# Kernel tuning notes

Hardware: AMD Instinct MI355X
Metric: run time of the kernel (lower is better)

## Reference

```python
import jax, jax.numpy as jnp
import numpy as np

N_NODES = 100000
N_SUPPORTS = 3
N_EDGES = 500000
D_IN = 128
D_OUT = 128


def setup_inputs() -> dict:
    key = jax.random.key(0)
    k1, k2, k3, k4, k5 = jax.random.split(key, 5)
    x = jax.random.normal(k1, (N_NODES, D_IN), dtype=jnp.float32)
    # glorot-ish scale for weights
    W = jax.random.normal(k2, (N_SUPPORTS, D_IN, D_OUT), dtype=jnp.float32) * np.sqrt(2.0 / (D_IN + D_OUT)).astype(np.float32)
    edge_src = jax.random.randint(k3, (N_SUPPORTS, N_EDGES), 0, N_NODES, dtype=jnp.int32)
    edge_dst = jax.random.randint(k4, (N_SUPPORTS, N_EDGES), 0, N_NODES, dtype=jnp.int32)
    edge_val = jax.random.uniform(k5, (N_SUPPORTS, N_EDGES), dtype=jnp.float32)
    return {"x": x, "W": W, "edge_src": edge_src, "edge_dst": edge_dst, "edge_val": edge_val}


def reference(x, W, edge_src, edge_dst, edge_val):
    """HMGConvolution forward (adj_power=1, multi_weight, no attention/reweight).

    x:        [N, Din] dense node features
    W:        [S, Din, Dout] per-support weights
    edge_src: [S, E] source node ids of each adjacency (COO)
    edge_dst: [S, E] destination node ids
    edge_val: [S, E] adjacency values
    Returns relu(sum_s  A_s @ (x @ W_s))  -> [N, Dout]
    """
    n_nodes = x.shape[0]
    # dense transform per support: [S, N, Dout]
    pre_sup = jnp.einsum('nd,sde->sne', x, W)

    def spmm(pre_s, src, dst, val):
        # messages gathered from source nodes, scaled by edge weight
        msgs = val[:, None] * pre_s[src]  # [E, Dout]
        return jax.ops.segment_sum(msgs, dst, num_segments=n_nodes)  # [N, Dout]

    supports = jax.vmap(spmm)(pre_sup, edge_src, edge_dst, edge_val)  # [S, N, Dout]
    return jax.nn.relu(jnp.sum(supports, axis=0))
```

## Files before the change

### kernel.cpp

```cpp
#include <hip/hip_runtime.h>

#define DIN 128
#define DOUT 128
#define EPB 4096
#define BKT 512
#define PACK_BITS 19
#define SRCG_MASK ((1u << PACK_BITS) - 1u)

typedef __attribute__((ext_vector_type(8))) short short8;
typedef __attribute__((ext_vector_type(4))) float f32x4;
typedef __attribute__((ext_vector_type(8))) unsigned short ushort8;

__device__ __forceinline__ unsigned short f2bf(float f) {
  unsigned int u = __float_as_uint(f);
  u += 0x7fffu + ((u >> 16) & 1u);
  return (unsigned short)(u >> 16);
}


__global__ __launch_bounds__(256) void wconvert(const float* __restrict__ W,
                                                unsigned short* __restrict__ wT) {
  __shared__ unsigned short buf[128][136];
  const int s = blockIdx.x;
  const float* Ws = W + (size_t)s * DIN * DOUT;
  unsigned short* wts = wT + (size_t)s * DIN * DOUT;
  const int tid = threadIdx.x;
#pragma unroll
  for (int i = 0; i < 16; ++i) {
    int e = tid + i * 256;
    int k = e >> 5, c = (e & 31) * 4;
    float4 v = *reinterpret_cast<const float4*>(&Ws[(size_t)k * DOUT + c]);
    buf[c][k] = f2bf(v.x); buf[c + 1][k] = f2bf(v.y);
    buf[c + 2][k] = f2bf(v.z); buf[c + 3][k] = f2bf(v.w);
  }
  __syncthreads();
#pragma unroll
  for (int i = 0; i < 8; ++i) {
    int e = tid + i * 256;
    int r = e >> 4, c = (e & 15) * 8;
    *reinterpret_cast<ushort8*>(&wts[(size_t)r * DIN + c]) =
        *reinterpret_cast<const ushort8*>(&buf[r][c]);
  }
}


__global__ __launch_bounds__(256) void gemm_mfma(const float* __restrict__ x,
                                                 const unsigned short* __restrict__ wT,
                                                 unsigned short* __restrict__ pre,
                                                 int n_nodes, int n_sup) {
  __shared__ unsigned short cst[128][136];

  const int tid = threadIdx.x;
  const int lane = tid & 63;
  const int w = tid >> 6;
  const int row0 = blockIdx.x * 128;
  const int alr = lane & 15;
  const int akg = lane >> 4;

  short8 afrag[4][2];
#pragma unroll
  for (int kc = 0; kc < 4; ++kc)
#pragma unroll
    for (int mt = 0; mt < 2; ++mt) {
      int gr = row0 + w * 32 + mt * 16 + alr;
      short8 a = {0, 0, 0, 0, 0, 0, 0, 0};
      if (gr < n_nodes) {
        const float4* p =
            reinterpret_cast<const float4*>(&x[(size_t)gr * DIN + kc * 32 + akg * 8]);
        float4 v0 = p[0];
        float4 v1 = p[1];
        a[0] = (short)f2bf(v0.x); a[1] = (short)f2bf(v0.y);
        a[2] = (short)f2bf(v0.z); a[3] = (short)f2bf(v0.w);
        a[4] = (short)f2bf(v1.x); a[5] = (short)f2bf(v1.y);
        a[6] = (short)f2bf(v1.z); a[7] = (short)f2bf(v1.w);
      }
      afrag[kc][mt] = a;
    }

  for (int s = 0; s < n_sup; ++s) {
    const unsigned short* wts = wT + (size_t)s * DIN * DOUT;

    f32x4 acc[2][8];
#pragma unroll
    for (int mt = 0; mt < 2; ++mt)
#pragma unroll
      for (int nt = 0; nt < 8; ++nt) acc[mt][nt] = (f32x4){0.f, 0.f, 0.f, 0.f};

#pragma unroll
    for (int kc = 0; kc < 4; ++kc) {
      short8 bfrag[8];
#pragma unroll
      for (int nt = 0; nt < 8; ++nt)
        bfrag[nt] = *reinterpret_cast<const short8*>(
            &wts[(size_t)(nt * 16 + alr) * DIN + kc * 32 + akg * 8]);
#pragma unroll
      for (int mt = 0; mt < 2; ++mt)
#pragma unroll
        for (int nt = 0; nt < 8; ++nt)
          acc[mt][nt] = __builtin_amdgcn_mfma_f32_16x16x32_bf16(
              afrag[kc][mt], bfrag[nt], acc[mt][nt], 0, 0, 0);
    }

    __syncthreads();
#pragma unroll
    for (int mt = 0; mt < 2; ++mt)
#pragma unroll
      for (int nt = 0; nt < 8; ++nt)
#pragma unroll
        for (int q = 0; q < 4; ++q)
          cst[w * 32 + mt * 16 + akg * 4 + q][nt * 16 + alr] = f2bf(acc[mt][nt][q]);
    __syncthreads();

    unsigned short* ps = pre + (size_t)s * n_nodes * DOUT;
#pragma unroll
    for (int i = 0; i < 8; ++i) {
      int e = tid + i * 256;
      int r = e >> 4;
      int c = (e & 15) * 8;
      int gr = row0 + r;
      if (gr < n_nodes)
        *reinterpret_cast<ushort8*>(&ps[(size_t)gr * DOUT + c]) =
            *reinterpret_cast<const ushort8*>(&cst[r][c]);
    }
  }
}


__global__ __launch_bounds__(256) void gemm_xw(const float* __restrict__ x,
                                               const float* __restrict__ W,
                                               float* __restrict__ pre,
                                               int n_nodes) {
  __shared__ float xsf[128][33];
  __shared__ float wtf[32][129];
  const float* Ws = W + (size_t)blockIdx.y * DIN * DOUT;
  float* pres = pre + (size_t)blockIdx.y * n_nodes * DOUT;
  const int tid = threadIdx.x;
  const int row0 = blockIdx.x * 128;
  const int tcol = tid & 15;
  const int trow = tid >> 4;
  float acc[8][8];
#pragma unroll
  for (int i = 0; i < 8; ++i)
#pragma unroll
    for (int j = 0; j < 8; ++j) acc[i][j] = 0.f;
#pragma unroll 1
  for (int kk = 0; kk < DIN; kk += 32) {
#pragma unroll
    for (int i = 0; i < 4; ++i) {
      int e = tid + i * 256;
      int r = e >> 3, c = (e & 7) * 4;
      int gr = row0 + r;
      float4 v = make_float4(0.f, 0.f, 0.f, 0.f);
      if (gr < n_nodes)
        v = *reinterpret_cast<const float4*>(&x[(size_t)gr * DIN + kk + c]);
      xsf[r][c] = v.x; xsf[r][c + 1] = v.y; xsf[r][c + 2] = v.z; xsf[r][c + 3] = v.w;
    }
#pragma unroll
    for (int i = 0; i < 4; ++i) {
      int e = tid + i * 256;
      int k = e >> 5, c = (e & 31) * 4;
      float4 v = *reinterpret_cast<const float4*>(&Ws[(size_t)(kk + k) * DOUT + c]);
      wtf[k][c] = v.x; wtf[k][c + 1] = v.y; wtf[k][c + 2] = v.z; wtf[k][c + 3] = v.w;
    }
    __syncthreads();
#pragma unroll 4
    for (int k = 0; k < 32; ++k) {
      float a[8], b[8];
#pragma unroll
      for (int i = 0; i < 8; ++i) a[i] = xsf[trow * 8 + i][k];
#pragma unroll
      for (int j = 0; j < 8; ++j) b[j] = wtf[k][tcol + 16 * j];
#pragma unroll
      for (int i = 0; i < 8; ++i)
#pragma unroll
        for (int j = 0; j < 8; ++j) acc[i][j] = fmaf(a[i], b[j], acc[i][j]);
    }
    __syncthreads();
  }
#pragma unroll
  for (int i = 0; i < 8; ++i) {
    int gr = row0 + trow * 8 + i;
    if (gr < n_nodes) {
#pragma unroll
      for (int j = 0; j < 8; ++j)
        pres[(size_t)gr * DOUT + tcol + 16 * j] = acc[i][j];
    }
  }
}


__global__ __launch_bounds__(256) void bucket_count(const int* __restrict__ dst_all,
                                                    int* __restrict__ bucket_cnt, int TE) {
  __shared__ int cnt[256];
  const int tid = threadIdx.x;
  cnt[tid] = 0;
  __syncthreads();
  const int beg = blockIdx.x * EPB;
  const int end = min(beg + EPB, TE);
  for (int i = beg + tid; i < end; i += 256) atomicAdd(&cnt[dst_all[i] >> 9], 1);
  __syncthreads();
  int c = cnt[tid];
  if (c) atomicAdd(&bucket_cnt[tid], c);
}

__global__ __launch_bounds__(256) void bucket_scan(const int* __restrict__ bucket_cnt,
                                                   int* __restrict__ bucket_base,
                                                   int* __restrict__ bucket_cursor,
                                                   int NB, int TE) {
  __shared__ int tmp[256];
  const int tid = threadIdx.x;
  int v = (tid < NB) ? bucket_cnt[tid] : 0;
  tmp[tid] = v;
  __syncthreads();
#pragma unroll
  for (int d = 1; d < 256; d <<= 1) {
    int t = (tid >= d) ? tmp[tid - d] : 0;
    __syncthreads();
    tmp[tid] += t;
    __syncthreads();
  }
  int excl = tmp[tid] - v;
  if (tid < NB) {
    bucket_base[tid] = excl;
    bucket_cursor[tid] = excl;
  }
  if (tid == 0) bucket_base[NB] = TE;
}

__global__ __launch_bounds__(256) void partition_edges(const int* __restrict__ src_all,
                                                       const int* __restrict__ dst_all,
                                                       const float* __restrict__ val_all,
                                                       int* __restrict__ bucket_cursor,
                                                       int2* __restrict__ part,
                                                       int TE, int n_nodes, int n_edges) {
  __shared__ int cnt[256];
  __shared__ int base_l[256];
  const int tid = threadIdx.x;
  const int beg = blockIdx.x * EPB;
  const int end = min(beg + EPB, TE);

  cnt[tid] = 0;
  __syncthreads();
  for (int i = beg + tid; i < end; i += 256) atomicAdd(&cnt[dst_all[i] >> 9], 1);
  __syncthreads();

  int c = cnt[tid];
  int mybase = (c > 0) ? atomicAdd(&bucket_cursor[tid], c) : 0;
  __syncthreads();
  base_l[tid] = mybase;
  cnt[tid] = 0;
  __syncthreads();

  for (int i = beg + tid; i < end; i += 256) {
    int d = dst_all[i];
    int b = d >> 9;
    int r = atomicAdd(&cnt[b], 1);
    int s = i / n_edges;
    unsigned key = (unsigned)(s * n_nodes + src_all[i]) |
                   ((unsigned)(d & (BKT - 1)) << PACK_BITS);
    part[base_l[b] + r] = make_int2((int)key, __float_as_int(val_all[i]));
  }
}

__global__ __launch_bounds__(256) void csr_build(const int2* __restrict__ part,
                                                 const int* __restrict__ bucket_base,
                                                 int2* __restrict__ csr,
                                                 int* __restrict__ row_off,
                                                 int n_nodes, int TE) {
  __shared__ int cnt[BKT];
  __shared__ int off_s[BKT];
  __shared__ int tmp[256];
  const int b = blockIdx.x;
  const int tid = threadIdx.x;
  const int bb = bucket_base[b];
  const int be = bucket_base[b + 1];

  cnt[tid] = 0;
  cnt[tid + 256] = 0;
  __syncthreads();
  for (int j = bb + tid; j < be; j += 256)
    atomicAdd(&cnt[((unsigned)part[j].x) >> PACK_BITS], 1);
  __syncthreads();

  int s2 = cnt[2 * tid] + cnt[2 * tid + 1];
  tmp[tid] = s2;
  __syncthreads();
#pragma unroll
  for (int d = 1; d < 256; d <<= 1) {
    int t = (tid >= d) ? tmp[tid - d] : 0;
    __syncthreads();
    tmp[tid] += t;
    __syncthreads();
  }
  int excl2 = tmp[tid] - s2;
  off_s[2 * tid] = excl2;
  off_s[2 * tid + 1] = excl2 + cnt[2 * tid];
  __syncthreads();

#pragma unroll
  for (int k = tid; k < BKT; k += 256) {
    int node = b * BKT + k;
    if (node < n_nodes) row_off[node] = bb + off_s[k];
  }
  cnt[tid] = off_s[tid];
  cnt[tid + 256] = off_s[tid + 256];
  __syncthreads();

  for (int j = bb + tid; j < be; j += 256) {
    int2 e = part[j];
    int dl = ((unsigned)e.x) >> PACK_BITS;
    int p = bb + atomicAdd(&cnt[dl], 1);
    csr[p] = e;
  }
  if (b == 0 && tid == 0) row_off[n_nodes] = TE;
}


__global__ __launch_bounds__(256) void spmm_gather8(const unsigned short* __restrict__ pre,
                                                    const int2* __restrict__ csr,
                                                    const int* __restrict__ row_off,
                                                    float* __restrict__ out, int n_nodes) {
  const int lane = threadIdx.x & 63;
  const int g = lane >> 3;
  const int t = lane & 7;
  const int wave = blockIdx.x * (blockDim.x >> 6) + (threadIdx.x >> 6);
  const int nwaves = gridDim.x * (blockDim.x >> 6);

  for (int n = wave; n < n_nodes; n += nwaves) {
    const int beg = row_off[n];
    const int end = row_off[n + 1];
    float acc[16];
#pragma unroll
    for (int k = 0; k < 16; ++k) acc[k] = 0.f;

    for (int j = beg + g; j < end; j += 8) {
      const int2 e = csr[j];
      const float v = __int_as_float(e.y);
      const unsigned srcg = ((unsigned)e.x) & SRCG_MASK;
      const ushort8* pr =
          reinterpret_cast<const ushort8*>(&pre[(size_t)srcg * DOUT + t * 16]);
      ushort8 p0 = pr[0];
      ushort8 p1 = pr[1];
#pragma unroll
      for (int k = 0; k < 8; ++k) {
        acc[k]     = fmaf(v, __uint_as_float((unsigned int)(unsigned short)p0[k] << 16), acc[k]);
        acc[8 + k] = fmaf(v, __uint_as_float((unsigned int)(unsigned short)p1[k] << 16), acc[8 + k]);
      }
    }

#pragma unroll
    for (int d = 8; d <= 32; d <<= 1)
#pragma unroll
      for (int k = 0; k < 16; ++k) acc[k] += __shfl_xor(acc[k], d, 64);

    float r0 = 0.f, r1 = 0.f;
#pragma unroll
    for (int gg = 0; gg < 8; ++gg)
      if (gg == g) { r0 = acc[gg * 2]; r1 = acc[gg * 2 + 1]; }
    r0 = fmaxf(r0, 0.f);
    r1 = fmaxf(r1, 0.f);
    *reinterpret_cast<float2*>(&out[(size_t)n * DOUT + t * 16 + g * 2]) =
        make_float2(r0, r1);
  }
}


__global__ __launch_bounds__(256) void edge_hist(const int* __restrict__ dst_base,
                                                 int* __restrict__ counts,
                                                 int n_edges, int n_nodes) {
  int i = blockIdx.x * blockDim.x + threadIdx.x;
  int s = blockIdx.y;
  if (i < n_edges) atomicAdd(&counts[s * n_nodes + dst_base[(size_t)s * n_edges + i]], 1);
}

__global__ __launch_bounds__(256) void scan_local(const int* __restrict__ counts,
                                                  int* __restrict__ row_off,
                                                  int* __restrict__ partials, int n) {
  __shared__ int tmp[256];
  const int tid = threadIdx.x;
  const int base = blockIdx.x * 2048 + tid * 8;
  int v[8];
#pragma unroll
  for (int i = 0; i < 8; ++i) v[i] = (base + i < n) ? counts[base + i] : 0;
  int s = 0;
#pragma unroll
  for (int i = 0; i < 8; ++i) s += v[i];
  tmp[tid] = s;
  __syncthreads();
#pragma unroll
  for (int d = 1; d < 256; d <<= 1) {
    int t = (tid >= d) ? tmp[tid - d] : 0;
    __syncthreads();
    tmp[tid] += t;
    __syncthreads();
  }
  int p = tmp[tid] - s;
#pragma unroll
  for (int i = 0; i < 8; ++i) {
    if (base + i < n) row_off[base + i] = p;
    p += v[i];
  }
  if (tid == 255) partials[blockIdx.x] = tmp[255];
}

__global__ __launch_bounds__(256) void scan_partials_k(int* __restrict__ partials, int nblk) {
  __shared__ int tmp[256];
  const int tid = threadIdx.x;
  int v = (tid < nblk) ? partials[tid] : 0;
  tmp[tid] = v;
  __syncthreads();
#pragma unroll
  for (int d = 1; d < 256; d <<= 1) {
    int t = (tid >= d) ? tmp[tid - d] : 0;
    __syncthreads();
    tmp[tid] += t;
    __syncthreads();
  }
  if (tid < nblk) partials[tid] = tmp[tid] - v;
}

__global__ __launch_bounds__(256) void scan_finish(int* __restrict__ row_off,
                                                   int* __restrict__ cursor,
                                                   const int* __restrict__ partials,
                                                   int n, int total_edges) {
  const int off = partials[blockIdx.x];
  const int base = blockIdx.x * 2048 + threadIdx.x * 8;
#pragma unroll
  for (int i = 0; i < 8; ++i) {
    int idx = base + i;
    if (idx < n) {
      int v = row_off[idx] + off;
      row_off[idx] = v;
      cursor[idx] = v;
    }
  }
  if (blockIdx.x == 0 && threadIdx.x == 0) row_off[n] = total_edges;
}

__global__ __launch_bounds__(256) void edge_fill(const int* __restrict__ src_base,
                                                 const int* __restrict__ dst_base,
                                                 const float* __restrict__ val_base,
                                                 int* __restrict__ cursor,
                                                 int2* __restrict__ csr,
                                                 int n_edges, int n_nodes) {
  int i = blockIdx.x * blockDim.x + threadIdx.x;
  int s = blockIdx.y;
  if (i < n_edges) {
    size_t gi = (size_t)s * n_edges + i;
    int d = dst_base[gi];
    int pos = atomicAdd(&cursor[s * n_nodes + d], 1);
    csr[pos] = make_int2(src_base[gi], __float_as_int(val_base[gi]));
  }
}

__global__ __launch_bounds__(256) void spmm_gather(const float* __restrict__ pre,
                                                   const int2* __restrict__ csr,
                                                   const int* __restrict__ row_off,
                                                   float* __restrict__ out,
                                                   int n_nodes, int n_sup, int mode) {
  const int lane = threadIdx.x & 63;
  const int wave = blockIdx.x * (blockDim.x >> 6) + (threadIdx.x >> 6);
  const int nwaves = gridDim.x * (blockDim.x >> 6);
  for (int n = wave; n < n_nodes; n += nwaves) {
    float ax = 0.f, ay = 0.f;
    float2* o = reinterpret_cast<float2*>(&out[(size_t)n * DOUT + lane * 2]);
    if (mode & 1) { float2 prev = *o; ax = prev.x; ay = prev.y; }
    for (int s = 0; s < n_sup; ++s) {
      const float* ps = pre + (size_t)s * n_nodes * DOUT;
      const int row = s * n_nodes + n;
      const int beg = row_off[row];
      const int end = row_off[row + 1];
      for (int j = beg; j < end; ++j) {
        const int2 e = csr[j];
        const float v = __int_as_float(e.y);
        const float2 p = *reinterpret_cast<const float2*>(&ps[(size_t)e.x * DOUT + lane * 2]);
        ax = fmaf(v, p.x, ax);
        ay = fmaf(v, p.y, ay);
      }
    }
    if (mode & 2) { ax = fmaxf(ax, 0.f); ay = fmaxf(ay, 0.f); }
    *o = make_float2(ax, ay);
  }
}

__global__ __launch_bounds__(256) void zero_f4(float4* __restrict__ p, int n4) {
  int i = blockIdx.x * blockDim.x + threadIdx.x;
  int stride = gridDim.x * blockDim.x;
  float4 z = make_float4(0.f, 0.f, 0.f, 0.f);
  for (; i < n4; i += stride) p[i] = z;
}

__global__ __launch_bounds__(256) void relu_f4(float4* __restrict__ p, int n4) {
  int i = blockIdx.x * blockDim.x + threadIdx.x;
  int stride = gridDim.x * blockDim.x;
  for (; i < n4; i += stride) {
    float4 v = p[i];
    v.x = fmaxf(v.x, 0.f); v.y = fmaxf(v.y, 0.f);
    v.z = fmaxf(v.z, 0.f); v.w = fmaxf(v.w, 0.f);
    p[i] = v;
  }
}

__global__ __launch_bounds__(256) void spmm_atomic(const float* __restrict__ pre,
                                                   const int* __restrict__ src,
                                                   const int* __restrict__ dst,
                                                   const float* __restrict__ val,
                                                   float* __restrict__ out,
                                                   int n_edges) {
  const int lane = threadIdx.x & 63;
  const int wave = blockIdx.x * (blockDim.x >> 6) + (threadIdx.x >> 6);
  const int nwaves = gridDim.x * (blockDim.x >> 6);
  for (int e = wave; e < n_edges; e += nwaves) {
    int s = src[e];
    int d = dst[e];
    float v = val[e];
    const float2 p = *reinterpret_cast<const float2*>(&pre[(size_t)s * DOUT + lane * 2]);
    float* o = &out[(size_t)d * DOUT + lane * 2];
    atomicAdd(o, v * p.x);
    atomicAdd(o + 1, v * p.y);
  }
}


static inline size_t align_up(size_t v, size_t a) { return (v + a - 1) & ~(a - 1); }

extern "C" void kernel_launch(void* const* d_in, const int* in_sizes, int n_in,
                              void* d_out, int out_size, void* d_ws, size_t ws_size,
                              hipStream_t stream) {
  const float* x     = (const float*)d_in[0];
  const float* W     = (const float*)d_in[1];
  const int*   esrc  = (const int*)d_in[2];
  const int*   edst  = (const int*)d_in[3];
  const float* eval_ = (const float*)d_in[4];
  float* out = (float*)d_out;

  const int n_nodes    = in_sizes[0] / DIN;
  const int n_supports = in_sizes[1] / (DIN * DOUT);
  const int n_edges    = in_sizes[2] / n_supports;

  const int gemm_blocks = (n_nodes + 127) / 128;
  const int edge_blocks = (n_edges + 255) / 256;
  const int gather_blocks = (n_nodes + 3) / 4;

  {
    const int NR = n_supports * n_nodes;
    const int TE = n_supports * n_edges;
    const int NB = (n_nodes + BKT - 1) / BKT;
    const int eb = (TE + EPB - 1) / EPB;
    char* w = (char*)d_ws;
    size_t off = 0;
    unsigned short* pre3 = (unsigned short*)(w + off); off += align_up((size_t)NR * DOUT * 2, 256);
    unsigned short* wT = (unsigned short*)(w + off);   off += align_up((size_t)n_supports * DIN * DOUT * 2, 256);
    int* row_off = (int*)(w + off);      off += align_up((size_t)(n_nodes + 1) * 4, 256);
    int2* part = (int2*)(w + off);       off += align_up((size_t)TE * 8, 256);
    int2* csr = (int2*)(w + off);        off += align_up((size_t)TE * 8, 256);
    int* bucket_cnt = (int*)(w + off);   off += align_up(256 * 4, 256);
    int* bucket_base = (int*)(w + off);  off += align_up(257 * 4, 256);
    int* bucket_cur = (int*)(w + off);   off += align_up(256 * 4, 256);

    const bool packable = (size_t)n_supports * n_nodes < (1u << PACK_BITS);

    if (off <= ws_size && NB <= 256 && packable) {
      wconvert<<<n_supports, 256, 0, stream>>>(W, wT);
      gemm_mfma<<<gemm_blocks, 256, 0, stream>>>(x, wT, pre3, n_nodes, n_supports);
      hipMemsetAsync(bucket_cnt, 0, 256 * 4, stream);
      bucket_count<<<eb, 256, 0, stream>>>(edst, bucket_cnt, TE);
      bucket_scan<<<1, 256, 0, stream>>>(bucket_cnt, bucket_base, bucket_cur, NB, TE);
      partition_edges<<<eb, 256, 0, stream>>>(esrc, edst, eval_, bucket_cur, part,
                                              TE, n_nodes, n_edges);
      csr_build<<<NB, 256, 0, stream>>>(part, bucket_base, csr, row_off, n_nodes, TE);
      spmm_gather8<<<gather_blocks, 256, 0, stream>>>(pre3, csr, row_off, out, n_nodes);
      return;
    }
  }

  {
    const int scan_blocks = (n_nodes + 2047) / 2048;
    char* w = (char*)d_ws;
    size_t off = 0;
    float* pre = (float*)(w + off);    off += align_up((size_t)n_nodes * DOUT * 4, 256);
    int* row_off = (int*)(w + off);    off += align_up((size_t)(n_nodes + 1) * 4, 256);
    int* cursor = (int*)(w + off);     off += align_up((size_t)n_nodes * 4, 256);
    int2* csr = (int2*)(w + off);      off += align_up((size_t)n_edges * 8, 256);
    int* partials = (int*)(w + off);   off += align_up(1024 * 4, 256);

    if (off <= ws_size && scan_blocks <= 256) {
      for (int s = 0; s < n_supports; ++s) {
        const int* src = esrc + (size_t)s * n_edges;
        const int* dst = edst + (size_t)s * n_edges;
        const float* val = eval_ + (size_t)s * n_edges;
        gemm_xw<<<dim3(gemm_blocks, 1), 256, 0, stream>>>(x, W + (size_t)s * DIN * DOUT,
                                                          pre, n_nodes);
        hipMemsetAsync(cursor, 0, (size_t)n_nodes * 4, stream);
        edge_hist<<<dim3(edge_blocks, 1), 256, 0, stream>>>(dst, cursor, n_edges, n_nodes);
        scan_local<<<scan_blocks, 256, 0, stream>>>(cursor, row_off, partials, n_nodes);
        scan_partials_k<<<1, 256, 0, stream>>>(partials, scan_blocks);
        scan_finish<<<scan_blocks, 256, 0, stream>>>(row_off, cursor, partials, n_nodes, n_edges);
        edge_fill<<<dim3(edge_blocks, 1), 256, 0, stream>>>(src, dst, val, cursor, csr,
                                                            n_edges, n_nodes);
        int mode = (s == 0) ? 0 : 1;
        if (s == n_supports - 1) mode |= 2;
        spmm_gather<<<gather_blocks, 256, 0, stream>>>(pre, csr, row_off, out,
                                                       n_nodes, 1, mode);
      }
      return;
    }
  }

  {
    float* pre = (float*)d_ws;
    if (ws_size < (size_t)n_nodes * DOUT * 4) return;
    const int n4 = out_size / 4;
    zero_f4<<<2048, 256, 0, stream>>>((float4*)out, n4);
    for (int s = 0; s < n_supports; ++s) {
      gemm_xw<<<dim3(gemm_blocks, 1), 256, 0, stream>>>(x, W + (size_t)s * DIN * DOUT,
                                                        pre, n_nodes);
      spmm_atomic<<<2048, 256, 0, stream>>>(pre, esrc + (size_t)s * n_edges,
                                            edst + (size_t)s * n_edges,
                                            eval_ + (size_t)s * n_edges, out, n_edges);
    }
    relu_f4<<<2048, 256, 0, stream>>>((float4*)out, n4);
  }
}
```

Measured before the change: 190.2 us.

## Fuse bucket counting into GEMM launch and bucket scan into partition kernel

The destination-bucket histogram now runs as extra blocks appended to the MFMA GEMM grid, so the count overlaps the dense transform instead of running as a separate launch. The single-block bucket scan is removed. Each partition block recomputes the 256-entry prefix sum redundantly and adds an atomic cursor offset from a zeroed array. This saves two kernel launches and their serialization, at the cost of a little redundant scan work per partition block.

```diff
diff --git a/kernel.cpp b/kernel.cpp
--- a/kernel.cpp
+++ b/kernel.cpp
@@ -44,13 +44,31 @@
 }
 
 
-__global__ __launch_bounds__(256) void gemm_mfma(const float* __restrict__ x,
-                                                 const unsigned short* __restrict__ wT,
-                                                 unsigned short* __restrict__ pre,
-                                                 int n_nodes, int n_sup) {
+__global__ __launch_bounds__(256) void gemm_mfma_count(const float* __restrict__ x,
+                                                       const unsigned short* __restrict__ wT,
+                                                       unsigned short* __restrict__ pre,
+                                                       const int* __restrict__ dst_all,
+                                                       int* __restrict__ bucket_cnt,
+                                                       int n_nodes, int n_sup, int TE,
+                                                       int gemm_blocks) {
   __shared__ unsigned short cst[128][136];
 
   const int tid = threadIdx.x;
+
+  if (blockIdx.x >= gemm_blocks) {
+    int* cnt = reinterpret_cast<int*>(&cst[0][0]);
+    cnt[tid] = 0;
+    __syncthreads();
+    const int cb = blockIdx.x - gemm_blocks;
+    const int beg = cb * EPB;
+    const int end = min(beg + EPB, TE);
+    for (int i = beg + tid; i < end; i += 256) atomicAdd(&cnt[dst_all[i] >> 9], 1);
+    __syncthreads();
+    int c = cnt[tid];
+    if (c) atomicAdd(&bucket_cnt[tid], c);
+    return;
+  }
+
   const int lane = tid & 63;
   const int w = tid >> 6;
   const int row0 = blockIdx.x * 128;
@@ -126,6 +144,166 @@
 }
 
 
+__global__ __launch_bounds__(256) void partition_edges2(const int* __restrict__ src_all,
+                                                        const int* __restrict__ dst_all,
+                                                        const float* __restrict__ val_all,
+                                                        const int* __restrict__ bucket_cnt,
+                                                        int* __restrict__ cursor0,
+                                                        int* __restrict__ bucket_base,
+                                                        int2* __restrict__ part,
+                                                        int TE, int n_nodes, int n_edges,
+                                                        int NB) {
+  __shared__ int cnt[256];
+  __shared__ int base_s[256];
+  __shared__ int tmp[256];
+  const int tid = threadIdx.x;
+  const int beg = blockIdx.x * EPB;
+  const int end = min(beg + EPB, TE);
+
+  int v = (tid < NB) ? bucket_cnt[tid] : 0;
+  tmp[tid] = v;
+  __syncthreads();
+#pragma unroll
+  for (int d = 1; d < 256; d <<= 1) {
+    int t = (tid >= d) ? tmp[tid - d] : 0;
+    __syncthreads();
+    tmp[tid] += t;
+    __syncthreads();
+  }
+  int excl = tmp[tid] - v;
+  base_s[tid] = excl;
+  if (blockIdx.x == 0) {
+    if (tid < NB) bucket_base[tid] = excl;
+    if (tid == 0) bucket_base[NB] = TE;
+  }
+
+  cnt[tid] = 0;
+  __syncthreads();
+  for (int i = beg + tid; i < end; i += 256) atomicAdd(&cnt[dst_all[i] >> 9], 1);
+  __syncthreads();
+
+  int c = cnt[tid];
+  int mybase = (c > 0) ? base_s[tid] + atomicAdd(&cursor0[tid], c) : 0;
+  __syncthreads();
+  tmp[tid] = mybase;
+  cnt[tid] = 0;
+  __syncthreads();
+
+  for (int i = beg + tid; i < end; i += 256) {
+    int d = dst_all[i];
+    int b = d >> 9;
+    int r = atomicAdd(&cnt[b], 1);
+    int s = i / n_edges;
+    unsigned key = (unsigned)(s * n_nodes + src_all[i]) |
+                   ((unsigned)(d & (BKT - 1)) << PACK_BITS);
+    part[tmp[b] + r] = make_int2((int)key, __float_as_int(val_all[i]));
+  }
+}
+
+
+__global__ __launch_bounds__(256) void csr_build(const int2* __restrict__ part,
+                                                 const int* __restrict__ bucket_base,
+                                                 int2* __restrict__ csr,
+                                                 int* __restrict__ row_off,
+                                                 int n_nodes, int TE) {
+  __shared__ int cnt[BKT];
+  __shared__ int off_s[BKT];
+  __shared__ int tmp[256];
+  const int b = blockIdx.x;
+  const int tid = threadIdx.x;
+  const int bb = bucket_base[b];
+  const int be = bucket_base[b + 1];
+
+  cnt[tid] = 0;
+  cnt[tid + 256] = 0;
+  __syncthreads();
+  for (int j = bb + tid; j < be; j += 256)
+    atomicAdd(&cnt[((unsigned)part[j].x) >> PACK_BITS], 1);
+  __syncthreads();
+
+  int s2 = cnt[2 * tid] + cnt[2 * tid + 1];
+  tmp[tid] = s2;
+  __syncthreads();
+#pragma unroll
+  for (int d = 1; d < 256; d <<= 1) {
+    int t = (tid >= d) ? tmp[tid - d] : 0;
+    __syncthreads();
+    tmp[tid] += t;
+    __syncthreads();
+  }
+  int excl2 = tmp[tid] - s2;
+  off_s[2 * tid] = excl2;
+  off_s[2 * tid + 1] = excl2 + cnt[2 * tid];
+  __syncthreads();
+
+#pragma unroll
+  for (int k = tid; k < BKT; k += 256) {
+    int node = b * BKT + k;
+    if (node < n_nodes) row_off[node] = bb + off_s[k];
+  }
+  cnt[tid] = off_s[tid];
+  cnt[tid + 256] = off_s[tid + 256];
+  __syncthreads();
+
+  for (int j = bb + tid; j < be; j += 256) {
+    int2 e = part[j];
+    int dl = ((unsigned)e.x) >> PACK_BITS;
+    int p = bb + atomicAdd(&cnt[dl], 1);
+    csr[p] = e;
+  }
+  if (b == 0 && tid == 0) row_off[n_nodes] = TE;
+}
+
+
+__global__ __launch_bounds__(256) void spmm_gather8(const unsigned short* __restrict__ pre,
+                                                    const int2* __restrict__ csr,
+                                                    const int* __restrict__ row_off,
+                                                    float* __restrict__ out, int n_nodes) {
+  const int lane = threadIdx.x & 63;
+  const int g = lane >> 3;
+  const int t = lane & 7;
+  const int wave = blockIdx.x * (blockDim.x >> 6) + (threadIdx.x >> 6);
+  const int nwaves = gridDim.x * (blockDim.x >> 6);
+
+  for (int n = wave; n < n_nodes; n += nwaves) {
+    const int beg = row_off[n];
+    const int end = row_off[n + 1];
+    float acc[16];
+#pragma unroll
+    for (int k = 0; k < 16; ++k) acc[k] = 0.f;
+
+    for (int j = beg + g; j < end; j += 8) {
+      const int2 e = csr[j];
+      const float v = __int_as_float(e.y);
+      const unsigned srcg = ((unsigned)e.x) & SRCG_MASK;
+      const ushort8* pr =
+          reinterpret_cast<const ushort8*>(&pre[(size_t)srcg * DOUT + t * 16]);
+      ushort8 p0 = pr[0];
+      ushort8 p1 = pr[1];
+#pragma unroll
+      for (int k = 0; k < 8; ++k) {
+        acc[k]     = fmaf(v, __uint_as_float((unsigned int)(unsigned short)p0[k] << 16), acc[k]);
+        acc[8 + k] = fmaf(v, __uint_as_float((unsigned int)(unsigned short)p1[k] << 16), acc[8 + k]);
+      }
+    }
+
+#pragma unroll
+    for (int d = 8; d <= 32; d <<= 1)
+#pragma unroll
+      for (int k = 0; k < 16; ++k) acc[k] += __shfl_xor(acc[k], d, 64);
+
+    float r0 = 0.f, r1 = 0.f;
+#pragma unroll
+    for (int gg = 0; gg < 8; ++gg)
+      if (gg == g) { r0 = acc[gg * 2]; r1 = acc[gg * 2 + 1]; }
+    r0 = fmaxf(r0, 0.f);
+    r1 = fmaxf(r1, 0.f);
+    *reinterpret_cast<float2*>(&out[(size_t)n * DOUT + t * 16 + g * 2]) =
+        make_float2(r0, r1);
+  }
+}
+
+
 __global__ __launch_bounds__(256) void gemm_xw(const float* __restrict__ x,
                                                const float* __restrict__ W,
                                                float* __restrict__ pre,
@@ -187,183 +365,6 @@
     }
   }
 }
-
-
-__global__ __launch_bounds__(256) void bucket_count(const int* __restrict__ dst_all,
-                                                    int* __restrict__ bucket_cnt, int TE) {
-  __shared__ int cnt[256];
-  const int tid = threadIdx.x;
-  cnt[tid] = 0;
-  __syncthreads();
-  const int beg = blockIdx.x * EPB;
-  const int end = min(beg + EPB, TE);
-  for (int i = beg + tid; i < end; i += 256) atomicAdd(&cnt[dst_all[i] >> 9], 1);
-  __syncthreads();
-  int c = cnt[tid];
-  if (c) atomicAdd(&bucket_cnt[tid], c);
-}
-
-__global__ __launch_bounds__(256) void bucket_scan(const int* __restrict__ bucket_cnt,
-                                                   int* __restrict__ bucket_base,
-                                                   int* __restrict__ bucket_cursor,
-                                                   int NB, int TE) {
-  __shared__ int tmp[256];
-  const int tid = threadIdx.x;
-  int v = (tid < NB) ? bucket_cnt[tid] : 0;
-  tmp[tid] = v;
-  __syncthreads();
-#pragma unroll
-  for (int d = 1; d < 256; d <<= 1) {
-    int t = (tid >= d) ? tmp[tid - d] : 0;
-    __syncthreads();
-    tmp[tid] += t;
-    __syncthreads();
-  }
-  int excl = tmp[tid] - v;
-  if (tid < NB) {
-    bucket_base[tid] = excl;
-    bucket_cursor[tid] = excl;
-  }
-  if (tid == 0) bucket_base[NB] = TE;
-}
-
-__global__ __launch_bounds__(256) void partition_edges(const int* __restrict__ src_all,
-                                                       const int* __restrict__ dst_all,
-                                                       const float* __restrict__ val_all,
-                                                       int* __restrict__ bucket_cursor,
-                                                       int2* __restrict__ part,
-                                                       int TE, int n_nodes, int n_edges) {
-  __shared__ int cnt[256];
-  __shared__ int base_l[256];
-  const int tid = threadIdx.x;
-  const int beg = blockIdx.x * EPB;
-  const int end = min(beg + EPB, TE);
-
-  cnt[tid] = 0;
-  __syncthreads();
-  for (int i = beg + tid; i < end; i += 256) atomicAdd(&cnt[dst_all[i] >> 9], 1);
-  __syncthreads();
-
-  int c = cnt[tid];
-  int mybase = (c > 0) ? atomicAdd(&bucket_cursor[tid], c) : 0;
-  __syncthreads();
-  base_l[tid] = mybase;
-  cnt[tid] = 0;
-  __syncthreads();
-
-  for (int i = beg + tid; i < end; i += 256) {
-    int d = dst_all[i];
-    int b = d >> 9;
-    int r = atomicAdd(&cnt[b], 1);
-    int s = i / n_edges;
-    unsigned key = (unsigned)(s * n_nodes + src_all[i]) |
-                   ((unsigned)(d & (BKT - 1)) << PACK_BITS);
-    part[base_l[b] + r] = make_int2((int)key, __float_as_int(val_all[i]));
-  }
-}
-
-__global__ __launch_bounds__(256) void csr_build(const int2* __restrict__ part,
-                                                 const int* __restrict__ bucket_base,
-                                                 int2* __restrict__ csr,
-                                                 int* __restrict__ row_off,
-                                                 int n_nodes, int TE) {
-  __shared__ int cnt[BKT];
-  __shared__ int off_s[BKT];
-  __shared__ int tmp[256];
-  const int b = blockIdx.x;
-  const int tid = threadIdx.x;
-  const int bb = bucket_base[b];
-  const int be = bucket_base[b + 1];
-
-  cnt[tid] = 0;
-  cnt[tid + 256] = 0;
-  __syncthreads();
-  for (int j = bb + tid; j < be; j += 256)
-    atomicAdd(&cnt[((unsigned)part[j].x) >> PACK_BITS], 1);
-  __syncthreads();
-
-  int s2 = cnt[2 * tid] + cnt[2 * tid + 1];
-  tmp[tid] = s2;
-  __syncthreads();
-#pragma unroll
-  for (int d = 1; d < 256; d <<= 1) {
-    int t = (tid >= d) ? tmp[tid - d] : 0;
-    __syncthreads();
-    tmp[tid] += t;
-    __syncthreads();
-  }
-  int excl2 = tmp[tid] - s2;
-  off_s[2 * tid] = excl2;
-  off_s[2 * tid + 1] = excl2 + cnt[2 * tid];
-  __syncthreads();
-
-#pragma unroll
-  for (int k = tid; k < BKT; k += 256) {
-    int node = b * BKT + k;
-    if (node < n_nodes) row_off[node] = bb + off_s[k];
-  }
-  cnt[tid] = off_s[tid];
-  cnt[tid + 256] = off_s[tid + 256];
-  __syncthreads();
-
-  for (int j = bb + tid; j < be; j += 256) {
-    int2 e = part[j];
-    int dl = ((unsigned)e.x) >> PACK_BITS;
-    int p = bb + atomicAdd(&cnt[dl], 1);
-    csr[p] = e;
-  }
-  if (b == 0 && tid == 0) row_off[n_nodes] = TE;
-}
-
-
-__global__ __launch_bounds__(256) void spmm_gather8(const unsigned short* __restrict__ pre,
-                                                    const int2* __restrict__ csr,
-                                                    const int* __restrict__ row_off,
-                                                    float* __restrict__ out, int n_nodes) {
-  const int lane = threadIdx.x & 63;
-  const int g = lane >> 3;
-  const int t = lane & 7;
-  const int wave = blockIdx.x * (blockDim.x >> 6) + (threadIdx.x >> 6);
-  const int nwaves = gridDim.x * (blockDim.x >> 6);
-
-  for (int n = wave; n < n_nodes; n += nwaves) {
-    const int beg = row_off[n];
-    const int end = row_off[n + 1];
-    float acc[16];
-#pragma unroll
-    for (int k = 0; k < 16; ++k) acc[k] = 0.f;
-
-    for (int j = beg + g; j < end; j += 8) {
-      const int2 e = csr[j];
-      const float v = __int_as_float(e.y);
-      const unsigned srcg = ((unsigned)e.x) & SRCG_MASK;
-      const ushort8* pr =
-          reinterpret_cast<const ushort8*>(&pre[(size_t)srcg * DOUT + t * 16]);
-      ushort8 p0 = pr[0];
-      ushort8 p1 = pr[1];
-#pragma unroll
-      for (int k = 0; k < 8; ++k) {
-        acc[k]     = fmaf(v, __uint_as_float((unsigned int)(unsigned short)p0[k] << 16), acc[k]);
-        acc[8 + k] = fmaf(v, __uint_as_float((unsigned int)(unsigned short)p1[k] << 16), acc[8 + k]);
-      }
-    }
-
-#pragma unroll
-    for (int d = 8; d <= 32; d <<= 1)
-#pragma unroll
-      for (int k = 0; k < 16; ++k) acc[k] += __shfl_xor(acc[k], d, 64);
-
-    float r0 = 0.f, r1 = 0.f;
-#pragma unroll
-    for (int gg = 0; gg < 8; ++gg)
-      if (gg == g) { r0 = acc[gg * 2]; r1 = acc[gg * 2 + 1]; }
-    r0 = fmaxf(r0, 0.f);
-    r1 = fmaxf(r1, 0.f);
-    *reinterpret_cast<float2*>(&out[(size_t)n * DOUT + t * 16 + g * 2]) =
-        make_float2(r0, r1);
-  }
-}
-
 
 __global__ __launch_bounds__(256) void edge_hist(const int* __restrict__ dst_base,
                                                  int* __restrict__ counts,
@@ -540,13 +541,13 @@
 
   const int gemm_blocks = (n_nodes + 127) / 128;
   const int edge_blocks = (n_edges + 255) / 256;
-  const int gather_blocks = (n_nodes + 3) / 4;
 
   {
     const int NR = n_supports * n_nodes;
     const int TE = n_supports * n_edges;
     const int NB = (n_nodes + BKT - 1) / BKT;
     const int eb = (TE + EPB - 1) / EPB;
+    const int gather_blocks = (n_nodes + 3) / 4;
     char* w = (char*)d_ws;
     size_t off = 0;
     unsigned short* pre3 = (unsigned short*)(w + off); off += align_up((size_t)NR * DOUT * 2, 256);
@@ -555,19 +556,18 @@
     int2* part = (int2*)(w + off);       off += align_up((size_t)TE * 8, 256);
     int2* csr = (int2*)(w + off);        off += align_up((size_t)TE * 8, 256);
     int* bucket_cnt = (int*)(w + off);   off += align_up(256 * 4, 256);
+    int* cursor0 = (int*)(w + off);      off += align_up(256 * 4, 256);
     int* bucket_base = (int*)(w + off);  off += align_up(257 * 4, 256);
-    int* bucket_cur = (int*)(w + off);   off += align_up(256 * 4, 256);
 
     const bool packable = (size_t)n_supports * n_nodes < (1u << PACK_BITS);
 
     if (off <= ws_size && NB <= 256 && packable) {
+      hipMemsetAsync(bucket_cnt, 0, 2 * 256 * 4, stream);
       wconvert<<<n_supports, 256, 0, stream>>>(W, wT);
-      gemm_mfma<<<gemm_blocks, 256, 0, stream>>>(x, wT, pre3, n_nodes, n_supports);
-      hipMemsetAsync(bucket_cnt, 0, 256 * 4, stream);
-      bucket_count<<<eb, 256, 0, stream>>>(edst, bucket_cnt, TE);
-      bucket_scan<<<1, 256, 0, stream>>>(bucket_cnt, bucket_base, bucket_cur, NB, TE);
-      partition_edges<<<eb, 256, 0, stream>>>(esrc, edst, eval_, bucket_cur, part,
-                                              TE, n_nodes, n_edges);
+      gemm_mfma_count<<<gemm_blocks + eb, 256, 0, stream>>>(
+          x, wT, pre3, edst, bucket_cnt, n_nodes, n_supports, TE, gemm_blocks);
+      partition_edges2<<<eb, 256, 0, stream>>>(esrc, edst, eval_, bucket_cnt, cursor0,
+                                               bucket_base, part, TE, n_nodes, n_edges, NB);
       csr_build<<<NB, 256, 0, stream>>>(part, bucket_base, csr, row_off, n_nodes, TE);
       spmm_gather8<<<gather_blocks, 256, 0, stream>>>(pre3, csr, row_off, out, n_nodes);
       return;
@@ -576,6 +576,7 @@
 
   {
     const int scan_blocks = (n_nodes + 2047) / 2048;
+    const int gather_blocks = (n_nodes + 3) / 4;
     char* w = (char*)d_ws;
     size_t off = 0;
     float* pre = (float*)(w + off);    off += align_up((size_t)n_nodes * DOUT * 4, 256);
```

New measurement: 183.2 us. 3.7% less time.
